# Performance work log

Hardware: AMD Instinct MI355X
Metric: run time of the kernel (lower is better)

Reference implementation:

```python
import jax, jax.numpy as jnp
import numpy as np

G = 7  # number of winner/loser assets

def setup_inputs() -> dict:
    key = jax.random.key(0)
    x = jax.random.normal(key, (4096, 8192, 1), dtype=jnp.float32)
    return {"x": x}

def reference(x):
    # x: [B, I, 1] -> [B, I]
    x = jnp.squeeze(x, axis=-1)
    # descending sort (argsort of -x gives descending order); gather values consistently
    sorted_indices = jnp.argsort(-x, axis=-1)                      # [B, I]
    sorted_x = jnp.take_along_axis(x, sorted_indices, axis=-1)     # [B, I] descending
    winner = jax.nn.softmax(sorted_x[:, :G], axis=-1)              # [B, G]
    loser = -jax.nn.softmax(1.0 - sorted_x[:, -G:], axis=-1)       # [B, G]
    zeros_mid = jnp.zeros_like(sorted_x[:, G:-G])                  # [B, I-2G]
    b_c = jnp.concatenate([winner, zeros_mid, loser], axis=1)      # [B, I]
    return (b_c, sorted_indices)
```

## Files before the change

### kernel.cpp

```cpp
#include <hip/hip_runtime.h>
#include <stdint.h>

#define N 8192
#define G 7
#define T 512
#define NW 8
typedef uint32_t u32;
typedef uint16_t u16;

__device__ __forceinline__ u32 enc_desc(float x) {
    u32 u = __float_as_uint(x);
    return (u & 0x80000000u) ? u : (~u & 0x7FFFFFFFu);
}
__device__ __forceinline__ float dec_desc(u32 k) {
    u32 u = (k & 0x80000000u) ? k : (~k & 0x7FFFFFFFu);
    return __uint_as_float(u);
}

__device__ __forceinline__ u32 dig_word(u32 d) { return (d & 127u) ^ ((d >> 7) * 0x2Bu); }
__device__ __forceinline__ u32 dig_col16(u32 d) { return (dig_word(d) << 1) | (d >> 7); }

__global__ __launch_bounds__(T) void portfolio_radix_kernel(
    const float* __restrict__ x,
    float* __restrict__ bc,
    float* __restrict__ idx_out)
{
    __shared__ u32 val_s[N];
    __shared__ u16 idx_s[N];
    __shared__ u32 wcnt32[NW * 128];
    __shared__ u32 wsum[4];

    const int t    = threadIdx.x;
    const int w    = t >> 6;
    const int lane = t & 63;
    const int row  = blockIdx.x;
    const float* xr  = x + (size_t)row * N;
    float* bcr = bc + (size_t)row * N;
    float* ixr = idx_out + (size_t)row * N;

    u16* wcnt16 = (u16*)wcnt32;

    u32 hi[16];
    u32 ii[16];
    u32 rnk[16];
#pragma unroll
    for (int j = 0; j < 16; ++j) {
        int e = (w << 10) | (j << 6) | lane;
        hi[j] = enc_desc(xr[e]);
        ii[j] = (u32)e;
        if (e >= G && e < N - G) bcr[e] = 0.0f;
    }
    wcnt32[(w << 7) + lane] = 0;
    wcnt32[(w << 7) + 64 + lane] = 0;

    for (int p = 0; p < 4; ++p) {
        const int shift = 8 * p;

#pragma unroll
        for (int j = 0; j < 16; ++j) {
            u32 d   = (hi[j] >> shift) & 255u;
            u32 sh  = (d >> 7) << 4;
            u32 ret = atomicAdd(&wcnt32[(w << 7) + dig_word(d)], 1u << sh);
            rnk[j]  = (ret >> sh) & 0xFFFFu;
        }
        __syncthreads();

        u32 vtot = 0, runv = 0;
        if (t < 256) {
            const int col = (int)dig_col16((u32)t);
            u32 run = 0;
#pragma unroll
            for (int ww = 0; ww < NW; ++ww) {
                u32 c = (u32)wcnt16[(ww << 8) + col];
                wcnt16[(ww << 8) + col] = (u16)run;
                run += c;
            }
            u32 v = run;
#pragma unroll
            for (int off = 1; off < 64; off <<= 1) {
                u32 u = __shfl_up(v, off, 64);
                if (lane >= off) v += u;
            }
            if (lane == 63) wsum[w] = v;
            vtot = v; runv = run;
        }
        __syncthreads();

        if (t < 256) {
            u32 dbase = vtot - runv;
            if (w > 0) dbase += wsum[0];
            if (w > 1) dbase += wsum[1];
            if (w > 2) dbase += wsum[2];
            const int col = (int)dig_col16((u32)t);
#pragma unroll
            for (int ww = 0; ww < NW; ++ww)
                wcnt16[(ww << 8) + col] = (u16)((u32)wcnt16[(ww << 8) + col] + dbase);
        }
        __syncthreads();

#pragma unroll
        for (int j = 0; j < 16; ++j) {
            u32 d   = (hi[j] >> shift) & 255u;
            u32 pos = rnk[j] + (u32)wcnt16[(w << 8) + dig_col16(d)];
            if (p < 3 || pos < G || pos >= N - G) val_s[pos] = hi[j];
            idx_s[pos] = (u16)ii[j];
        }
        asm volatile("" ::: "memory");
        wcnt32[(w << 7) + lane] = 0;
        wcnt32[(w << 7) + 64 + lane] = 0;
        __syncthreads();

        if (p < 3) {
#pragma unroll
            for (int j = 0; j < 16; ++j) {
                int e = (w << 10) | (j << 6) | lane;
                hi[j] = val_s[e];
                ii[j] = (u32)idx_s[e];
            }
        }
    }

#pragma unroll
    for (int j = 0; j < 16; ++j) {
        int e = (w << 10) | (j << 6) | lane;
        ixr[e] = (float)idx_s[e];
    }
    if (t < G) {
        float s[G], ex[G], sum = 0.f;
#pragma unroll
        for (int g = 0; g < G; ++g) s[g] = dec_desc(val_s[g]);
        float m0 = s[0];
#pragma unroll
        for (int g = 0; g < G; ++g) { ex[g] = expf(s[g] - m0); sum += ex[g]; }
        bcr[t] = ex[t] / sum;
    }
    if (t >= T - G) {
        float s[G], ex[G], sum = 0.f;
#pragma unroll
        for (int g = 0; g < G; ++g) s[g] = dec_desc(val_s[N - G + g]);
        float m0 = -s[G - 1];
#pragma unroll
        for (int g = 0; g < G; ++g) { ex[g] = expf(-s[g] - m0); sum += ex[g]; }
        bcr[(N - T) + t] = -ex[t - (T - G)] / sum;
    }
}

extern "C" void kernel_launch(void* const* d_in, const int* in_sizes, int n_in,
                              void* d_out, int out_size, void* d_ws, size_t ws_size,
                              hipStream_t stream) {
    const float* x = (const float*)d_in[0];
    float* out = (float*)d_out;
    const int B = in_sizes[0] / N;
    float* bc  = out;
    float* idx = out + (size_t)B * N;
    portfolio_radix_kernel<<<B, T, 0, stream>>>(x, bc, idx);
}
```

Baseline: 442.8 us.

## Double block threads to 1024 and merge scan base into scatter

Uses 16 waves per row, so each thread holds 8 keys instead of 16. Rank and source index are packed into one register. The next pass's reload is fused into the counting loop. The third barrier in each pass is removed by adding the chunk offsets during the scatter. The aim is more occupancy and latency hiding with fewer syncs, at the cost of a longer per-wave scan across 16 waves and more atomic contention per digit counter.

Result: slower. 520.3 us (+17.5%).

```diff
diff --git a/kernel.cpp b/kernel.cpp
--- a/kernel.cpp
+++ b/kernel.cpp
@@ -3,8 +3,8 @@
 
 #define N 8192
 #define G 7
-#define T 512
-#define NW 8
+#define T 1024
+#define NW 16
 typedef uint32_t u32;
 typedef uint16_t u16;
 
@@ -40,14 +40,12 @@
 
     u16* wcnt16 = (u16*)wcnt32;
 
-    u32 hi[16];
-    u32 ii[16];
-    u32 rnk[16];
+    u32 hi[8];
+    u32 rni[8];
 #pragma unroll
-    for (int j = 0; j < 16; ++j) {
-        int e = (w << 10) | (j << 6) | lane;
+    for (int j = 0; j < 8; ++j) {
+        int e = (w << 9) | (j << 6) | lane;
         hi[j] = enc_desc(xr[e]);
-        ii[j] = (u32)e;
         if (e >= G && e < N - G) bcr[e] = 0.0f;
     }
     wcnt32[(w << 7) + lane] = 0;
@@ -56,25 +54,37 @@
     for (int p = 0; p < 4; ++p) {
         const int shift = 8 * p;
 
+        if (p == 0) {
 #pragma unroll
-        for (int j = 0; j < 16; ++j) {
-            u32 d   = (hi[j] >> shift) & 255u;
-            u32 sh  = (d >> 7) << 4;
-            u32 ret = atomicAdd(&wcnt32[(w << 7) + dig_word(d)], 1u << sh);
-            rnk[j]  = (ret >> sh) & 0xFFFFu;
+            for (int j = 0; j < 8; ++j) {
+                int e   = (w << 9) | (j << 6) | lane;
+                u32 d   = hi[j] & 255u;
+                u32 sh  = (d >> 7) << 4;
+                u32 ret = atomicAdd(&wcnt32[(w << 7) + dig_word(d)], 1u << sh);
+                rni[j]  = ((ret >> sh) & 0xFFFFu) | ((u32)e << 16);
+            }
+        } else {
+#pragma unroll
+            for (int j = 0; j < 8; ++j) {
+                int e   = (w << 9) | (j << 6) | lane;
+                hi[j]   = val_s[e];
+                u32 iv  = (u32)idx_s[e];
+                u32 d   = (hi[j] >> shift) & 255u;
+                u32 sh  = (d >> 7) << 4;
+                u32 ret = atomicAdd(&wcnt32[(w << 7) + dig_word(d)], 1u << sh);
+                rni[j]  = ((ret >> sh) & 0xFFFFu) | (iv << 16);
+            }
         }
         __syncthreads();
 
-        u32 vtot = 0, runv = 0;
         if (t < 256) {
             const int col = (int)dig_col16((u32)t);
+            u32 c[NW];
+#pragma unroll
+            for (int ww = 0; ww < NW; ++ww) c[ww] = (u32)wcnt16[(ww << 8) + col];
             u32 run = 0;
 #pragma unroll
-            for (int ww = 0; ww < NW; ++ww) {
-                u32 c = (u32)wcnt16[(ww << 8) + col];
-                wcnt16[(ww << 8) + col] = (u16)run;
-                run += c;
-            }
+            for (int ww = 0; ww < NW; ++ww) { u32 cc = c[ww]; c[ww] = run; run += cc; }
             u32 v = run;
 #pragma unroll
             for (int off = 1; off < 64; off <<= 1) {
@@ -82,47 +92,35 @@
                 if (lane >= off) v += u;
             }
             if (lane == 63) wsum[w] = v;
-            vtot = v; runv = run;
+            u32 dbase = v - run;
+#pragma unroll
+            for (int ww = 0; ww < NW; ++ww)
+                wcnt16[(ww << 8) + col] = (u16)(c[ww] + dbase);
         }
         __syncthreads();
 
-        if (t < 256) {
-            u32 dbase = vtot - runv;
-            if (w > 0) dbase += wsum[0];
-            if (w > 1) dbase += wsum[1];
-            if (w > 2) dbase += wsum[2];
-            const int col = (int)dig_col16((u32)t);
+        {
+            u32 s0 = wsum[0], s1 = wsum[1], s2 = wsum[2];
 #pragma unroll
-            for (int ww = 0; ww < NW; ++ww)
-                wcnt16[(ww << 8) + col] = (u16)((u32)wcnt16[(ww << 8) + col] + dbase);
-        }
-        __syncthreads();
-
-#pragma unroll
-        for (int j = 0; j < 16; ++j) {
-            u32 d   = (hi[j] >> shift) & 255u;
-            u32 pos = rnk[j] + (u32)wcnt16[(w << 8) + dig_col16(d)];
-            if (p < 3 || pos < G || pos >= N - G) val_s[pos] = hi[j];
-            idx_s[pos] = (u16)ii[j];
+            for (int j = 0; j < 8; ++j) {
+                u32 d    = (hi[j] >> shift) & 255u;
+                u32 ch   = d >> 6;
+                u32 coff = (ch > 0 ? s0 : 0u) + (ch > 1 ? s1 : 0u) + (ch > 2 ? s2 : 0u);
+                u32 pos  = (rni[j] & 0xFFFFu)
+                         + (u32)wcnt16[(w << 8) + dig_col16(d)] + coff;
+                if (p < 3 || pos < G || pos >= N - G) val_s[pos] = hi[j];
+                idx_s[pos] = (u16)(rni[j] >> 16);
+            }
         }
         asm volatile("" ::: "memory");
         wcnt32[(w << 7) + lane] = 0;
         wcnt32[(w << 7) + 64 + lane] = 0;
         __syncthreads();
-
-        if (p < 3) {
-#pragma unroll
-            for (int j = 0; j < 16; ++j) {
-                int e = (w << 10) | (j << 6) | lane;
-                hi[j] = val_s[e];
-                ii[j] = (u32)idx_s[e];
-            }
-        }
     }
 
 #pragma unroll
-    for (int j = 0; j < 16; ++j) {
-        int e = (w << 10) | (j << 6) | lane;
+    for (int j = 0; j < 8; ++j) {
+        int e = (w << 9) | (j << 6) | lane;
         ixr[e] = (float)idx_s[e];
     }
     if (t < G) {
```
